# Performance work log

Hardware: AMD Instinct MI355X
Metric: run time of the kernel (lower is better)

The kernel has to match this reference:

```python
import jax, jax.numpy as jnp
import numpy as np
import math

CEN_W = 1.0
ANG_W = 1.0


def _radius(ndim):
    # Iterative version of the recursive Radius() from the source.
    if ndim < 1:
        raise ValueError('ndim >= 1 required')
    if ndim == 1:
        return 0.0
    r = 0.5
    for _ in range(3, ndim + 1):
        r = 0.5 / math.sqrt(1.0 - r * r)
    return r


def _costheta(ndim):
    return 2.0 * _radius(ndim - 1) ** 2 - 1.0


def setup_inputs() -> dict:
    key = jax.random.key(0)
    k1, k2, k3 = jax.random.split(key, 3)
    B, C, D = 65536, 1000, 512
    y = jax.random.randint(k1, (B,), 0, C, dtype=jnp.int64 if jax.config.jax_enable_x64 else jnp.int32)
    feat = jax.random.normal(k2, (B, D), dtype=jnp.float32)
    centers = jax.random.normal(k3, (C, D), dtype=jnp.float32)
    return {"y": y, "feat": feat, "centers": centers}


def reference(y, feat, centers):
    C = centers.shape[0]
    B = feat.shape[0]
    ct = jnp.float32(_costheta(C))  # static Python constant from num_classes

    # ---- center loss: gather assigned centers, squared diff sum ----
    centers_pred = centers[y]                      # [B, D] gather
    diff = feat - centers_pred
    loss_cen = 0.5 * jnp.sum(diff * diff) / B

    # ---- angular loss: vectorized Gram matrix over classes ----
    # In torch, centers[j].data and dist are detached -> stop_gradient here.
    centers_sg = jax.lax.stop_gradient(centers)
    dist = jnp.linalg.norm(centers_sg, axis=1)     # [C], detached
    gram = centers @ centers_sg.T                  # [C, C]; grad flows via rows only
    sim = gram / (dist[:, None] * dist[None, :])
    offdiag = 1.0 - jnp.eye(C, dtype=sim.dtype)
    loss_ang = jnp.sum(offdiag * (sim - ct) ** 2) / (0.5 * C * (C - 1))

    return loss_cen * CEN_W + loss_ang * ANG_W
```

## Files before the change

### kernel.cpp

```cpp
#include <hip/hip_runtime.h>
#include <math.h>

typedef __attribute__((ext_vector_type(8))) short bf16x8;
typedef __attribute__((ext_vector_type(4))) float f32x4;
typedef __attribute__((ext_vector_type(4))) float vf4;
typedef __attribute__((ext_vector_type(4))) unsigned int u32x4;

__device__ __forceinline__ float wave_reduce(float v) {
#pragma unroll
    for (int off = 32; off > 0; off >>= 1) v += __shfl_down(v, off, 64);
    return v;
}

__device__ __forceinline__ unsigned int pk_trunc(float f0, float f1) {
    unsigned u0 = __float_as_uint(f0), u1 = __float_as_uint(f1);
    return (u1 & 0xFFFF0000u) | (u0 >> 16);
}

__global__ __launch_bounds__(256) void fused_kernel(const int* __restrict__ y,
                                                    const vf4* __restrict__ feat4,
                                                    const vf4* __restrict__ cent4,
                                                    float* __restrict__ partials,
                                                    int n4, int d4, float cen_scale,
                                                    int C, int ntile, int steps,
                                                    float ct, float ang_scale) {
    const int bid = blockIdx.x;
    const int lane = threadIdx.x & 63;
    const int wid = threadIdx.x >> 6;
    __shared__ float sm[4];

    float partial = 0.f;

    const int t = bid * 4 + wid;
    const int ntile2 = ntile * ntile;
    if (t < ntile2) {
        const int ti = t / ntile;
        const int tj = t - ti * ntile;
        const int n = lane & 15;
        const int quad = lane >> 4;
        const int ra = ti * 16 + n;
        const int rb = tj * 16 + n;
        const bool va = ra < C;
        const bool vb = rb < C;
        const vf4* aptr = cent4 + (size_t)ra * d4 + quad * 2;
        const vf4* bptr = cent4 + (size_t)rb * d4 + quad * 2;
        f32x4 acc = {0.f, 0.f, 0.f, 0.f};
        float sa = 0.f, sb = 0.f;
#pragma unroll 4
        for (int st = 0; st < steps; ++st) {
            vf4 a0 = {0.f, 0.f, 0.f, 0.f}, a1 = a0, b0 = a0, b1 = a0;
            if (va) { a0 = aptr[st * 8]; a1 = aptr[st * 8 + 1]; }
            if (vb) { b0 = bptr[st * 8]; b1 = bptr[st * 8 + 1]; }
            sa += a0.x * a0.x + a0.y * a0.y + a0.z * a0.z + a0.w * a0.w
                + a1.x * a1.x + a1.y * a1.y + a1.z * a1.z + a1.w * a1.w;
            sb += b0.x * b0.x + b0.y * b0.y + b0.z * b0.z + b0.w * b0.w
                + b1.x * b1.x + b1.y * b1.y + b1.z * b1.z + b1.w * b1.w;
            u32x4 ap, bp;
            ap.x = pk_trunc(a0.x, a0.y); ap.y = pk_trunc(a0.z, a0.w);
            ap.z = pk_trunc(a1.x, a1.y); ap.w = pk_trunc(a1.z, a1.w);
            bp.x = pk_trunc(b0.x, b0.y); bp.y = pk_trunc(b0.z, b0.w);
            bp.z = pk_trunc(b1.x, b1.y); bp.w = pk_trunc(b1.z, b1.w);
            bf16x8 af = __builtin_bit_cast(bf16x8, ap);
            bf16x8 bf = __builtin_bit_cast(bf16x8, bp);
            acc = __builtin_amdgcn_mfma_f32_16x16x32_bf16(af, bf, acc, 0, 0, 0);
        }
        sa += __shfl_xor(sa, 16, 64); sa += __shfl_xor(sa, 32, 64);
        sb += __shfl_xor(sb, 16, 64); sb += __shfl_xor(sb, 32, 64);
        float di[4];
#pragma unroll
        for (int rr = 0; rr < 4; ++rr) di[rr] = __shfl(sa, quad * 4 + rr, 64);
        const int gj = tj * 16 + n;
        const float dj = sb;
        float local = 0.f;
#pragma unroll
        for (int rr = 0; rr < 4; ++rr) {
            const int gi = ti * 16 + quad * 4 + rr;
            if (gi < C && gj < C && gi != gj) {
                float sim = acc[rr] * rsqrtf(di[rr] * dj);
                float dlt = sim - ct;
                local += dlt * dlt;
            }
        }
        partial = local * ang_scale;
    }

    {
        const int stride = gridDim.x * 256;
        float s = 0.f;
        int i = bid * 256 + threadIdx.x;
        if ((stride % d4) == 0) {
            if (i < n4) {
                int row = i / d4;
                const int col = i - row * d4;
                const int rstep = stride / d4;
                for (; i < n4; i += stride, row += rstep) {
                    const int cls = y[row];
                    vf4 f = __builtin_nontemporal_load(feat4 + i);
                    vf4 c = cent4[(size_t)cls * d4 + col];
                    float dx = f.x - c.x, dy = f.y - c.y, dz = f.z - c.z, dw = f.w - c.w;
                    s += dx * dx + dy * dy + dz * dz + dw * dw;
                }
            }
        } else {
            for (; i < n4; i += stride) {
                int row = i / d4;
                int col = i - row * d4;
                const int cls = y[row];
                vf4 f = __builtin_nontemporal_load(feat4 + i);
                vf4 c = cent4[(size_t)cls * d4 + col];
                float dx = f.x - c.x, dy = f.y - c.y, dz = f.z - c.z, dw = f.w - c.w;
                s += dx * dx + dy * dy + dz * dz + dw * dw;
            }
        }
        partial += s * cen_scale;
    }

    float r = wave_reduce(partial);
    if (lane == 0) sm[wid] = r;
    __syncthreads();
    if (threadIdx.x == 0) {
        partials[bid] = sm[0] + sm[1] + sm[2] + sm[3];
    }
}

__global__ __launch_bounds__(256) void reduce_kernel(const float* __restrict__ partials,
                                                     float* __restrict__ out, int nb) {
    __shared__ float sm[4];
    const int lane = threadIdx.x & 63;
    const int wid = threadIdx.x >> 6;
    float s = 0.f;
    for (int i = threadIdx.x; i < nb; i += 256) s += partials[i];
    s = wave_reduce(s);
    if (lane == 0) sm[wid] = s;
    __syncthreads();
    if (threadIdx.x == 0) out[0] = sm[0] + sm[1] + sm[2] + sm[3];
}

extern "C" void kernel_launch(void* const* d_in, const int* in_sizes, int n_in,
                              void* d_out, int out_size, void* d_ws, size_t ws_size,
                              hipStream_t stream) {
    const int* y = (const int*)d_in[0];
    const float* feat = (const float*)d_in[1];
    const float* centers = (const float*)d_in[2];

    const int B = in_sizes[0];
    const int D = in_sizes[1] / B;
    const int C = in_sizes[2] / D;
    const int d4 = D / 4;
    const int ntile = (C + 15) / 16;

    const int nd = C - 1;
    double r = 0.0;
    if (nd >= 2) {
        r = 0.5;
        for (int i = 3; i <= nd; ++i) r = 0.5 / sqrt(1.0 - r * r);
    }
    const float ct = (float)(2.0 * r * r - 1.0);

    const float cen_scale = (float)(0.5 / (double)B);
    const float ang_scale = (float)(1.0 / (0.5 * (double)C * (double)(C - 1)));

    float* partials = (float*)d_ws;
    const int nb = 2048;

    fused_kernel<<<nb, 256, 0, stream>>>(
        y, (const vf4*)feat, (const vf4*)centers, partials,
        B * d4, d4, cen_scale, C, ntile, D / 32, ct, ang_scale);

    reduce_kernel<<<1, 256, 0, stream>>>(partials, (float*)d_out, nb);
}
```

Baseline: 214.7 us.

## Interleave Gram-matrix MFMA steps with center-loss streaming in one loop

Merges the angular-loss MFMA loop and the center-loss grid-stride loop into a single loop, so waves that own a Gram tile issue their MFMA step and their feat/center loads in the same iteration. Previously those waves ran the whole Gram tile before starting their streaming share, which serialized them behind the other waves. Also adds a min-blocks hint of 8 to launch_bounds to push occupancy up. The cost is extra per-iteration branching and more live registers, which the occupancy hint may force into spills.

```diff
diff --git a/kernel.cpp b/kernel.cpp
--- a/kernel.cpp
+++ b/kernel.cpp
@@ -17,37 +17,53 @@
     return (u1 & 0xFFFF0000u) | (u0 >> 16);
 }
 
-__global__ __launch_bounds__(256) void fused_kernel(const int* __restrict__ y,
-                                                    const vf4* __restrict__ feat4,
-                                                    const vf4* __restrict__ cent4,
-                                                    float* __restrict__ partials,
-                                                    int n4, int d4, float cen_scale,
-                                                    int C, int ntile, int steps,
-                                                    float ct, float ang_scale) {
+__global__ __launch_bounds__(256, 8) void fused_kernel(const int* __restrict__ y,
+                                                       const vf4* __restrict__ feat4,
+                                                       const vf4* __restrict__ cent4,
+                                                       float* __restrict__ partials,
+                                                       int n4, int d4, float cen_scale,
+                                                       int C, int ntile, int steps,
+                                                       float ct, float ang_scale) {
     const int bid = blockIdx.x;
     const int lane = threadIdx.x & 63;
     const int wid = threadIdx.x >> 6;
     __shared__ float sm[4];
 
-    float partial = 0.f;
-
     const int t = bid * 4 + wid;
     const int ntile2 = ntile * ntile;
-    if (t < ntile2) {
-        const int ti = t / ntile;
-        const int tj = t - ti * ntile;
-        const int n = lane & 15;
-        const int quad = lane >> 4;
+    const bool hasTile = (t < ntile2);
+    int ti = 0, tj = 0;
+    const int n = lane & 15;
+    const int quad = lane >> 4;
+    const vf4* aptr = cent4;
+    const vf4* bptr = cent4;
+    bool va = false, vb = false;
+    if (hasTile) {
+        ti = t / ntile;
+        tj = t - ti * ntile;
         const int ra = ti * 16 + n;
         const int rb = tj * 16 + n;
-        const bool va = ra < C;
-        const bool vb = rb < C;
-        const vf4* aptr = cent4 + (size_t)ra * d4 + quad * 2;
-        const vf4* bptr = cent4 + (size_t)rb * d4 + quad * 2;
-        f32x4 acc = {0.f, 0.f, 0.f, 0.f};
-        float sa = 0.f, sb = 0.f;
-#pragma unroll 4
-        for (int st = 0; st < steps; ++st) {
+        va = ra < C;
+        vb = rb < C;
+        aptr = cent4 + (size_t)ra * d4 + quad * 2;
+        bptr = cent4 + (size_t)rb * d4 + quad * 2;
+    }
+    f32x4 acc = {0.f, 0.f, 0.f, 0.f};
+    float sa = 0.f, sb = 0.f;
+
+    const int stride = gridDim.x * 256;
+    float cs = 0.f;
+    int i = bid * 256 + threadIdx.x;
+    int row = i / d4;
+    int col = i - row * d4;
+    const int rstep = stride / d4;
+    const bool colfast = (stride % d4) == 0;
+
+    const int citers = (i < n4) ? ((n4 - 1 - i) / stride + 1) : 0;
+    const int itmax = (steps > citers) ? steps : citers;
+    int st = 0;
+    for (int it = 0; it < itmax; ++it) {
+        if (hasTile && st < steps) {
             vf4 a0 = {0.f, 0.f, 0.f, 0.f}, a1 = a0, b0 = a0, b1 = a0;
             if (va) { a0 = aptr[st * 8]; a1 = aptr[st * 8 + 1]; }
             if (vb) { b0 = bptr[st * 8]; b1 = bptr[st * 8 + 1]; }
@@ -63,7 +79,23 @@
             bf16x8 af = __builtin_bit_cast(bf16x8, ap);
             bf16x8 bf = __builtin_bit_cast(bf16x8, bp);
             acc = __builtin_amdgcn_mfma_f32_16x16x32_bf16(af, bf, acc, 0, 0, 0);
+            ++st;
         }
+        if (i < n4) {
+            const int cls = y[row];
+            vf4 f = __builtin_nontemporal_load(feat4 + i);
+            vf4 c = cent4[(size_t)cls * d4 + col];
+            float dx = f.x - c.x, dy = f.y - c.y, dz = f.z - c.z, dw = f.w - c.w;
+            cs += dx * dx + dy * dy + dz * dz + dw * dw;
+            i += stride;
+            if (colfast) { row += rstep; }
+            else { row = i / d4; col = i - row * d4; }
+        }
+    }
+
+    float partial = cs * cen_scale;
+
+    if (hasTile) {
         sa += __shfl_xor(sa, 16, 64); sa += __shfl_xor(sa, 32, 64);
         sb += __shfl_xor(sb, 16, 64); sb += __shfl_xor(sb, 32, 64);
         float di[4];
@@ -81,38 +113,7 @@
                 local += dlt * dlt;
             }
         }
-        partial = local * ang_scale;
-    }
-
-    {
-        const int stride = gridDim.x * 256;
-        float s = 0.f;
-        int i = bid * 256 + threadIdx.x;
-        if ((stride % d4) == 0) {
-            if (i < n4) {
-                int row = i / d4;
-                const int col = i - row * d4;
-                const int rstep = stride / d4;
-                for (; i < n4; i += stride, row += rstep) {
-                    const int cls = y[row];
-                    vf4 f = __builtin_nontemporal_load(feat4 + i);
-                    vf4 c = cent4[(size_t)cls * d4 + col];
-                    float dx = f.x - c.x, dy = f.y - c.y, dz = f.z - c.z, dw = f.w - c.w;
-                    s += dx * dx + dy * dy + dz * dz + dw * dw;
-                }
-            }
-        } else {
-            for (; i < n4; i += stride) {
-                int row = i / d4;
-                int col = i - row * d4;
-                const int cls = y[row];
-                vf4 f = __builtin_nontemporal_load(feat4 + i);
-                vf4 c = cent4[(size_t)cls * d4 + col];
-                float dx = f.x - c.x, dy = f.y - c.y, dz = f.z - c.z, dw = f.w - c.w;
-                s += dx * dx + dy * dy + dz * dz + dw * dw;
-            }
-        }
-        partial += s * cen_scale;
+        partial += local * ang_scale;
     }
 
     float r = wave_reduce(partial);
```

Result: no change. 213.0 us (-0.8%).
